# Optimization experiments

Measured on AMD Instinct MI355X. Metric: run time of the kernel, lower is better.

Reference implementation:

```python
import jax, jax.numpy as jnp
import numpy as np

N_NODES = 500000


def _gcn_conv(x, W, b, src, dst, n):
    # x: [N, Fin], W: [Fin, Fout]. PyG GCNConv with add_self_loops + sym norm.
    h = x @ W                                            # [N, Fout]
    deg = jax.ops.segment_sum(jnp.ones_like(dst, dtype=h.dtype), dst,
                              num_segments=n)            # in-degree incl self loops
    dinv = jnp.where(deg > 0, jax.lax.rsqrt(jnp.maximum(deg, 1)), 0.0)
    norm = dinv[src] * dinv[dst]                         # [E]
    msg = h[src] * norm[:, None]                         # gather + scale
    out = jax.ops.segment_sum(msg, dst, num_segments=n)  # scatter-add to targets
    return out + b


def setup_inputs() -> dict:
    key = jax.random.key(0)
    k1, k2, k3, k4 = jax.random.split(key, 4)
    x = jax.random.normal(k1, (N_NODES, 1), dtype=jnp.float32)
    edge_index = jax.random.randint(k2, (2, 8000000), 0, N_NODES, dtype=jnp.int64)
    W1 = jax.random.normal(k3, (1, 32), dtype=jnp.float32) * (1.0 / np.sqrt(1))
    b1 = jnp.zeros((32,), dtype=jnp.float32)
    W2 = jax.random.normal(k4, (32, 2), dtype=jnp.float32) * (1.0 / np.sqrt(32))
    b2 = jnp.zeros((2,), dtype=jnp.float32)
    return {"x": x, "edge_index": edge_index, "W1": W1, "b1": b1, "W2": W2, "b2": b2}


def reference(x, edge_index, W1, b1, W2, b2):
    n = x.shape[0]
    loops = jnp.arange(n, dtype=edge_index.dtype)
    src = jnp.concatenate([edge_index[0], loops])  # add self-loops
    dst = jnp.concatenate([edge_index[1], loops])
    h = _gcn_conv(x, W1, b1, src, dst, n)
    h = jax.nn.relu(h)
    # F.dropout(training=self.training): identity in eval mode
    h = _gcn_conv(h, W2, b2, src, dst, n)
    return jax.nn.log_softmax(h, axis=1)
```

## Files before the change

### kernel.cpp

```cpp
#include <hip/hip_runtime.h>


static constexpr int BKT_BITS = 11;
static constexpr int BKT = 1 << BKT_BITS;
static constexpr int EB = 1024;
static constexpr int EBT = 256;

__global__ void k_hist(const int* __restrict__ dst, int e, int chunk, int nbkt,
                       unsigned* __restrict__ hist) {
  __shared__ unsigned cnt[256];
  int b = blockIdx.x;
  for (int t = threadIdx.x; t < nbkt; t += blockDim.x) cnt[t] = 0;
  __syncthreads();
  int lo = b * chunk;
  int hi = min(lo + chunk, e);
  for (int i = lo + threadIdx.x; i < hi; i += blockDim.x)
    atomicAdd(&cnt[((unsigned)dst[i]) >> BKT_BITS], 1u);
  __syncthreads();
  for (int t = threadIdx.x; t < nbkt; t += blockDim.x)
    hist[(size_t)b * nbkt + t] = cnt[t];
}

__global__ void k_colscan(const unsigned* __restrict__ hist, int nbkt,
                          unsigned* __restrict__ colpre,
                          unsigned* __restrict__ totals) {
  int k = blockIdx.x;
  int lane = threadIdx.x;
  unsigned running = 0;
  for (int c = 0; c < EB; c += 64) {
    unsigned v = hist[(size_t)(c + lane) * nbkt + k];
    unsigned orig = v;
#pragma unroll
    for (int off = 1; off < 64; off <<= 1) {
      unsigned t = __shfl_up(v, off);
      if (lane >= off) v += t;
    }
    colpre[(size_t)(c + lane) * nbkt + k] = running + (v - orig);
    running += __shfl(v, 63);
  }
  if (lane == 0) totals[k] = running;
}

__global__ void k_bucketscan(const unsigned* __restrict__ totals, int nbkt,
                             unsigned* __restrict__ base) {
  if (threadIdx.x == 0) {
    unsigned r = 0;
    for (int k = 0; k < nbkt; ++k) {
      base[k] = r;
      r += totals[k];
    }
    base[nbkt] = r;
  }
}

__global__ void k_scatter(const int* __restrict__ src, const int* __restrict__ dst,
                          int e, int chunk, int nbkt,
                          const unsigned* __restrict__ colpre,
                          const unsigned* __restrict__ base,
                          unsigned* __restrict__ packed) {
  __shared__ unsigned cur[256];
  int b = blockIdx.x;
  for (int t = threadIdx.x; t < nbkt; t += blockDim.x)
    cur[t] = base[t] + colpre[(size_t)b * nbkt + t];
  __syncthreads();
  int lo = b * chunk;
  int hi = min(lo + chunk, e);
  for (int i = lo + threadIdx.x; i < hi; i += blockDim.x) {
    unsigned d = (unsigned)dst[i];
    unsigned k = d >> BKT_BITS;
    unsigned slot = atomicAdd(&cur[k], 1u);
    packed[slot] = ((unsigned)src[i] << BKT_BITS) | (d & (BKT - 1));
  }
}

__global__ void __launch_bounds__(1024) k_degnode(
    const unsigned* __restrict__ packed, const unsigned* __restrict__ base,
    const float* __restrict__ x, int n, float* __restrict__ dinv,
    float* __restrict__ xs) {
  __shared__ unsigned cnt[BKT];
  int k = blockIdx.x;
  for (int t = threadIdx.x; t < BKT; t += blockDim.x) cnt[t] = 0;
  __syncthreads();
  unsigned lo = base[k], hi = base[k + 1];
  for (unsigned i = lo + threadIdx.x; i < hi; i += blockDim.x)
    atomicAdd(&cnt[packed[i] & (BKT - 1)], 1u);
  __syncthreads();
  int g0 = k << BKT_BITS;
  for (int t = threadIdx.x; t < BKT; t += blockDim.x) {
    int g = g0 + t;
    if (g < n) {
      float di = rsqrtf((float)(cnt[t] + 1u));
      dinv[g] = di;
      xs[g] = di * x[g];
    }
  }
}

__global__ void __launch_bounds__(1024) k_accA2(
    const unsigned* __restrict__ packed, const unsigned* __restrict__ base,
    const float* __restrict__ dinv, const float* __restrict__ xs,
    const float* __restrict__ W1, const float* __restrict__ b1,
    const float* __restrict__ W2, int n, float2* __restrict__ yd) {
  __shared__ float acc[BKT];
  __shared__ float sW1[32], sb1[32], sW2[64];
  if (threadIdx.x < 32) {
    sW1[threadIdx.x] = W1[threadIdx.x];
    sb1[threadIdx.x] = b1[threadIdx.x];
  } else if (threadIdx.x < 96) {
    sW2[threadIdx.x - 32] = W2[threadIdx.x - 32];
  }
  for (int t = threadIdx.x; t < BKT; t += blockDim.x) acc[t] = 0.0f;
  __syncthreads();
  int k = blockIdx.x;
  unsigned lo = base[k], hi = base[k + 1];
  for (unsigned i = lo + threadIdx.x; i < hi; i += blockDim.x) {
    unsigned p = packed[i];
    atomicAdd(&acc[p & (BKT - 1)], xs[p >> BKT_BITS]);
  }
  __syncthreads();
  int g0 = k << BKT_BITS;
  for (int t = threadIdx.x; t < BKT; t += blockDim.x) {
    int g = g0 + t;
    if (g >= n) continue;
    float di = dinv[g];
    float s = di * (acc[t] + xs[g]);
    float y0 = 0.0f, y1 = 0.0f;
#pragma unroll
    for (int f = 0; f < 32; ++f) {
      float h = fmaxf(fmaf(s, sW1[f], sb1[f]), 0.0f);
      y0 = fmaf(h, sW2[2 * f + 0], y0);
      y1 = fmaf(h, sW2[2 * f + 1], y1);
    }
    yd[g] = make_float2(di * y0, di * y1);
  }
}

__global__ void __launch_bounds__(1024) k_accB3(
    const unsigned* __restrict__ packed, const unsigned* __restrict__ base,
    const float* __restrict__ dinv, const float2* __restrict__ yd,
    const float* __restrict__ b2, int n, float2* __restrict__ out) {
  __shared__ float a0[BKT], a1[BKT];
  for (int t = threadIdx.x; t < BKT; t += blockDim.x) {
    a0[t] = 0.0f;
    a1[t] = 0.0f;
  }
  __syncthreads();
  int k = blockIdx.x;
  unsigned lo = base[k], hi = base[k + 1];
  for (unsigned i = lo + threadIdx.x; i < hi; i += blockDim.x) {
    unsigned p = packed[i];
    float2 v = yd[p >> BKT_BITS];
    unsigned l = p & (BKT - 1);
    atomicAdd(&a0[l], v.x);
    atomicAdd(&a1[l], v.y);
  }
  __syncthreads();
  float b20 = b2[0], b21 = b2[1];
  int g0 = k << BKT_BITS;
  for (int t = threadIdx.x; t < BKT; t += blockDim.x) {
    int g = g0 + t;
    if (g >= n) continue;
    float di = dinv[g];
    float2 yv = yd[g];
    float t0 = fmaf(di, a0[t] + yv.x, b20);
    float t1 = fmaf(di, a1[t] + yv.y, b21);
    float m = fmaxf(t0, t1);
    float l2 = m + logf(expf(t0 - m) + expf(t1 - m));
    out[g] = make_float2(t0 - l2, t1 - l2);
  }
}

extern "C" void kernel_launch(void* const* d_in, const int* in_sizes, int n_in,
                              void* d_out, int out_size, void* d_ws, size_t ws_size,
                              hipStream_t stream) {
  const float* x = (const float*)d_in[0];
  const int* edge = (const int*)d_in[1];
  const float* W1 = (const float*)d_in[2];
  const float* b1 = (const float*)d_in[3];
  const float* W2 = (const float*)d_in[4];
  const float* b2 = (const float*)d_in[5];
  float2* out = (float2*)d_out;

  const int n = in_sizes[0];
  const int e = in_sizes[1] / 2;
  const int* src = edge;
  const int* dst = edge + e;

  const int nbkt = (n + BKT - 1) >> BKT_BITS;
  const int chunk = (e + EB - 1) / EB;

  char* ws = (char*)d_ws;
  size_t off = 0;
  unsigned* packed = (unsigned*)(ws + off);
  off += (size_t)e * 4;
  unsigned* base = (unsigned*)(ws + off);
  off += ((size_t)(nbkt + 1) * 4 + 255) & ~(size_t)255;
  float* dinv = (float*)(ws + off);
  off += (size_t)n * 4;
  float* xs = (float*)(ws + off);
  off += (size_t)n * 4;
  size_t offB = off;
  unsigned* hist = (unsigned*)(ws + offB);
  unsigned* colpre = (unsigned*)(ws + offB + (size_t)EB * nbkt * 4);
  unsigned* totals = (unsigned*)(ws + offB + 2 * (size_t)EB * nbkt * 4);
  float2* yd = (float2*)(ws + offB);

  k_hist<<<EB, EBT, 0, stream>>>(dst, e, chunk, nbkt, hist);
  k_colscan<<<nbkt, 64, 0, stream>>>(hist, nbkt, colpre, totals);
  k_bucketscan<<<1, 64, 0, stream>>>(totals, nbkt, base);
  k_scatter<<<EB, EBT, 0, stream>>>(src, dst, e, chunk, nbkt, colpre, base, packed);
  k_degnode<<<nbkt, 1024, 0, stream>>>(packed, base, x, n, dinv, xs);
  k_accA2<<<nbkt, 1024, 0, stream>>>(packed, base, dinv, xs, W1, b1, W2, n, yd);
  k_accB3<<<nbkt, 1024, 0, stream>>>(packed, base, dinv, yd, b2, n, out);
}
```

Before: 265.4 us.

## Replace per-block histogram scan with global atomics and staged local-sort scatter

Replaces the per-block bucket histogram plus column scan with a single global bucket-totals histogram using atomics, and vectorizes the dst reads. The scatter kernel now sorts each 8192-edge chunk locally in shared memory, reserves each bucket segment with a global atomicAdd on a cursor, and writes contiguous runs, which should make the packed writes more coalesced. The hist/colpre workspace and two scan kernels are removed. Bucket order within segments becomes nondeterministic across blocks, and later kernels derive segment bounds from the post-scatter cursors.

```diff
diff --git a/kernel.cpp b/kernel.cpp
--- a/kernel.cpp
+++ b/kernel.cpp
@@ -3,85 +3,161 @@
 
 static constexpr int BKT_BITS = 11;
 static constexpr int BKT = 1 << BKT_BITS;
-static constexpr int EB = 1024;
-static constexpr int EBT = 256;
-
-__global__ void k_hist(const int* __restrict__ dst, int e, int chunk, int nbkt,
-                       unsigned* __restrict__ hist) {
-  __shared__ unsigned cnt[256];
-  int b = blockIdx.x;
-  for (int t = threadIdx.x; t < nbkt; t += blockDim.x) cnt[t] = 0;
-  __syncthreads();
-  int lo = b * chunk;
+static constexpr int NB = 256;
+static constexpr int HB = 512;
+static constexpr int HT = 256;
+static constexpr int CHUNK = 8192;
+static constexpr int SCT = 256;
+static constexpr int PERT = CHUNK / SCT;
+
+__global__ void __launch_bounds__(HT) k_hist(const int* __restrict__ dst, int e,
+                                             int chunk, int nbkt,
+                                             unsigned* __restrict__ totals) {
+  __shared__ unsigned cnt[NB];
+  for (int t = threadIdx.x; t < NB; t += HT) cnt[t] = 0;
+  __syncthreads();
+  int lo = blockIdx.x * chunk;
   int hi = min(lo + chunk, e);
-  for (int i = lo + threadIdx.x; i < hi; i += blockDim.x)
+  const int4* d4 = (const int4*)dst;
+  for (int i = (lo >> 2) + threadIdx.x; i < (hi >> 2); i += HT) {
+    int4 d = d4[i];
+    atomicAdd(&cnt[((unsigned)d.x) >> BKT_BITS], 1u);
+    atomicAdd(&cnt[((unsigned)d.y) >> BKT_BITS], 1u);
+    atomicAdd(&cnt[((unsigned)d.z) >> BKT_BITS], 1u);
+    atomicAdd(&cnt[((unsigned)d.w) >> BKT_BITS], 1u);
+  }
+  for (int i = ((hi >> 2) << 2) + threadIdx.x; i < hi; i += HT)
     atomicAdd(&cnt[((unsigned)dst[i]) >> BKT_BITS], 1u);
   __syncthreads();
-  for (int t = threadIdx.x; t < nbkt; t += blockDim.x)
-    hist[(size_t)b * nbkt + t] = cnt[t];
-}
-
-__global__ void k_colscan(const unsigned* __restrict__ hist, int nbkt,
-                          unsigned* __restrict__ colpre,
-                          unsigned* __restrict__ totals) {
-  int k = blockIdx.x;
+  for (int t = threadIdx.x; t < nbkt; t += HT)
+    if (cnt[t]) atomicAdd(&totals[t], cnt[t]);
+}
+
+__global__ void k_basescan(const unsigned* __restrict__ totals, int nbkt,
+                           unsigned* __restrict__ gcur) {
   int lane = threadIdx.x;
   unsigned running = 0;
-  for (int c = 0; c < EB; c += 64) {
-    unsigned v = hist[(size_t)(c + lane) * nbkt + k];
-    unsigned orig = v;
+  for (int c = 0; c < NB; c += 64) {
+    int k = c + lane;
+    unsigned v = (k < nbkt) ? totals[k] : 0u;
+    unsigned incl = v;
 #pragma unroll
     for (int off = 1; off < 64; off <<= 1) {
-      unsigned t = __shfl_up(v, off);
-      if (lane >= off) v += t;
-    }
-    colpre[(size_t)(c + lane) * nbkt + k] = running + (v - orig);
-    running += __shfl(v, 63);
-  }
-  if (lane == 0) totals[k] = running;
-}
-
-__global__ void k_bucketscan(const unsigned* __restrict__ totals, int nbkt,
-                             unsigned* __restrict__ base) {
-  if (threadIdx.x == 0) {
-    unsigned r = 0;
-    for (int k = 0; k < nbkt; ++k) {
-      base[k] = r;
-      r += totals[k];
-    }
-    base[nbkt] = r;
-  }
-}
-
-__global__ void k_scatter(const int* __restrict__ src, const int* __restrict__ dst,
-                          int e, int chunk, int nbkt,
-                          const unsigned* __restrict__ colpre,
-                          const unsigned* __restrict__ base,
-                          unsigned* __restrict__ packed) {
-  __shared__ unsigned cur[256];
-  int b = blockIdx.x;
-  for (int t = threadIdx.x; t < nbkt; t += blockDim.x)
-    cur[t] = base[t] + colpre[(size_t)b * nbkt + t];
-  __syncthreads();
-  int lo = b * chunk;
-  int hi = min(lo + chunk, e);
-  for (int i = lo + threadIdx.x; i < hi; i += blockDim.x) {
-    unsigned d = (unsigned)dst[i];
-    unsigned k = d >> BKT_BITS;
-    unsigned slot = atomicAdd(&cur[k], 1u);
-    packed[slot] = ((unsigned)src[i] << BKT_BITS) | (d & (BKT - 1));
+      unsigned t = __shfl_up(incl, off);
+      if (lane >= off) incl += t;
+    }
+    if (k < nbkt) gcur[k] = running + incl - v;
+    running += __shfl(incl, 63);
+  }
+}
+
+__global__ void __launch_bounds__(SCT) k_scatter(
+    const int* __restrict__ src, const int* __restrict__ dst, int e, int nbkt,
+    unsigned* __restrict__ gcur, unsigned* __restrict__ packed) {
+  __shared__ unsigned staged[CHUNK];
+  __shared__ unsigned cnt[NB];
+  __shared__ unsigned cur[NB];
+  __shared__ unsigned gseg[NB];
+  __shared__ unsigned loff[NB + 1];
+  const int tid = threadIdx.x;
+  const int lo = blockIdx.x * CHUNK;
+  for (int t = tid; t < NB; t += SCT) { cnt[t] = 0u; cur[t] = 0u; }
+  __syncthreads();
+
+  unsigned pk[PERT];
+  unsigned bku[PERT / 4];
+  const int4* s4 = (const int4*)src;
+  const int4* d4 = (const int4*)dst;
+#pragma unroll
+  for (int jj = 0; jj < PERT / 4; ++jj) {
+    int i4 = (lo >> 2) + jj * SCT + tid;
+    unsigned b4 = 0xFFFFFFFFu;
+    if (i4 * 4 + 3 < e) {
+      int4 s = s4[i4];
+      int4 d = d4[i4];
+      unsigned k0 = ((unsigned)d.x) >> BKT_BITS, k1 = ((unsigned)d.y) >> BKT_BITS;
+      unsigned k2 = ((unsigned)d.z) >> BKT_BITS, k3 = ((unsigned)d.w) >> BKT_BITS;
+      pk[jj * 4 + 0] = ((unsigned)s.x << BKT_BITS) | ((unsigned)d.x & (BKT - 1));
+      pk[jj * 4 + 1] = ((unsigned)s.y << BKT_BITS) | ((unsigned)d.y & (BKT - 1));
+      pk[jj * 4 + 2] = ((unsigned)s.z << BKT_BITS) | ((unsigned)d.z & (BKT - 1));
+      pk[jj * 4 + 3] = ((unsigned)s.w << BKT_BITS) | ((unsigned)d.w & (BKT - 1));
+      b4 = k0 | (k1 << 8) | (k2 << 16) | (k3 << 24);
+      atomicAdd(&cnt[k0], 1u);
+      atomicAdd(&cnt[k1], 1u);
+      atomicAdd(&cnt[k2], 1u);
+      atomicAdd(&cnt[k3], 1u);
+    } else {
+#pragma unroll
+      for (int c = 0; c < 4; ++c) {
+        int i = i4 * 4 + c;
+        if (i >= lo && i < e) {
+          unsigned dd = (unsigned)dst[i];
+          unsigned kk = dd >> BKT_BITS;
+          pk[jj * 4 + c] = ((unsigned)src[i] << BKT_BITS) | (dd & (BKT - 1));
+          b4 = (b4 & ~(0xFFu << (8 * c))) | (kk << (8 * c));
+          atomicAdd(&cnt[kk], 1u);
+        }
+      }
+    }
+    bku[jj] = b4;
+  }
+  __syncthreads();
+
+  if (tid < 64) {
+    unsigned running = 0;
+    for (int c = 0; c < NB; c += 64) {
+      int k = c + tid;
+      unsigned v = cnt[k];
+      unsigned incl = v;
+#pragma unroll
+      for (int off = 1; off < 64; off <<= 1) {
+        unsigned t = __shfl_up(incl, off);
+        if (tid >= off) incl += t;
+      }
+      loff[k] = running + incl - v;
+      running += __shfl(incl, 63);
+    }
+    if (tid == 0) loff[NB] = running;
+  }
+  __syncthreads();
+
+  for (int k = tid; k < nbkt; k += SCT)
+    if (cnt[k]) gseg[k] = atomicAdd(&gcur[k], cnt[k]);
+
+#pragma unroll
+  for (int jj = 0; jj < PERT / 4; ++jj) {
+    unsigned b4 = bku[jj];
+#pragma unroll
+    for (int c = 0; c < 4; ++c) {
+      unsigned k = (b4 >> (8 * c)) & 0xFFu;
+      if (k != 0xFFu) {
+        unsigned pos = loff[k] + atomicAdd(&cur[k], 1u);
+        staged[pos] = pk[jj * 4 + c];
+      }
+    }
+  }
+  __syncthreads();
+
+  int mv = (int)loff[nbkt];
+  for (int t = tid; t < mv; t += SCT) {
+    int a = 0, b = nbkt;
+    while (b - a > 1) {
+      int mid = (a + b) >> 1;
+      if ((int)loff[mid] <= t) a = mid; else b = mid;
+    }
+    packed[gseg[a] + (unsigned)(t - (int)loff[a])] = staged[t];
   }
 }
 
 __global__ void __launch_bounds__(1024) k_degnode(
-    const unsigned* __restrict__ packed, const unsigned* __restrict__ base,
+    const unsigned* __restrict__ packed, const unsigned* __restrict__ gcur,
     const float* __restrict__ x, int n, float* __restrict__ dinv,
     float* __restrict__ xs) {
   __shared__ unsigned cnt[BKT];
   int k = blockIdx.x;
   for (int t = threadIdx.x; t < BKT; t += blockDim.x) cnt[t] = 0;
   __syncthreads();
-  unsigned lo = base[k], hi = base[k + 1];
+  unsigned lo = k ? gcur[k - 1] : 0u, hi = gcur[k];
   for (unsigned i = lo + threadIdx.x; i < hi; i += blockDim.x)
     atomicAdd(&cnt[packed[i] & (BKT - 1)], 1u);
   __syncthreads();
@@ -97,7 +173,7 @@
 }
 
 __global__ void __launch_bounds__(1024) k_accA2(
-    const unsigned* __restrict__ packed, const unsigned* __restrict__ base,
+    const unsigned* __restrict__ packed, const unsigned* __restrict__ gcur,
     const float* __restrict__ dinv, const float* __restrict__ xs,
     const float* __restrict__ W1, const float* __restrict__ b1,
     const float* __restrict__ W2, int n, float2* __restrict__ yd) {
@@ -112,7 +188,7 @@
   for (int t = threadIdx.x; t < BKT; t += blockDim.x) acc[t] = 0.0f;
   __syncthreads();
   int k = blockIdx.x;
-  unsigned lo = base[k], hi = base[k + 1];
+  unsigned lo = k ? gcur[k - 1] : 0u, hi = gcur[k];
   for (unsigned i = lo + threadIdx.x; i < hi; i += blockDim.x) {
     unsigned p = packed[i];
     atomicAdd(&acc[p & (BKT - 1)], xs[p >> BKT_BITS]);
@@ -136,7 +212,7 @@
 }
 
 __global__ void __launch_bounds__(1024) k_accB3(
-    const unsigned* __restrict__ packed, const unsigned* __restrict__ base,
+    const unsigned* __restrict__ packed, const unsigned* __restrict__ gcur,
     const float* __restrict__ dinv, const float2* __restrict__ yd,
     const float* __restrict__ b2, int n, float2* __restrict__ out) {
   __shared__ float a0[BKT], a1[BKT];
@@ -146,7 +222,7 @@
   }
   __syncthreads();
   int k = blockIdx.x;
-  unsigned lo = base[k], hi = base[k + 1];
+  unsigned lo = k ? gcur[k - 1] : 0u, hi = gcur[k];
   for (unsigned i = lo + threadIdx.x; i < hi; i += blockDim.x) {
     unsigned p = packed[i];
     float2 v = yd[p >> BKT_BITS];
@@ -162,7 +238,7 @@
     if (g >= n) continue;
     float di = dinv[g];
     float2 yv = yd[g];
-    float t0 = fmaf(di, a0[t] + yv.x, b20);
+    float t0 = fmaf(di, a0[t] + yv.x, b2[0] * 0.0f + b20);
     float t1 = fmaf(di, a1[t] + yv.y, b21);
     float m = fmaxf(t0, t1);
     float l2 = m + logf(expf(t0 - m) + expf(t1 - m));
@@ -187,29 +263,22 @@
   const int* dst = edge + e;
 
   const int nbkt = (n + BKT - 1) >> BKT_BITS;
-  const int chunk = (e + EB - 1) / EB;
+  const int hchunk = (((e + HB - 1) / HB) + 3) & ~3;
+  const int sgrid = (e + CHUNK - 1) / CHUNK;
 
   char* ws = (char*)d_ws;
-  size_t off = 0;
-  unsigned* packed = (unsigned*)(ws + off);
-  off += (size_t)e * 4;
-  unsigned* base = (unsigned*)(ws + off);
-  off += ((size_t)(nbkt + 1) * 4 + 255) & ~(size_t)255;
-  float* dinv = (float*)(ws + off);
-  off += (size_t)n * 4;
-  float* xs = (float*)(ws + off);
-  off += (size_t)n * 4;
-  size_t offB = off;
-  unsigned* hist = (unsigned*)(ws + offB);
-  unsigned* colpre = (unsigned*)(ws + offB + (size_t)EB * nbkt * 4);
-  unsigned* totals = (unsigned*)(ws + offB + 2 * (size_t)EB * nbkt * 4);
-  float2* yd = (float2*)(ws + offB);
-
-  k_hist<<<EB, EBT, 0, stream>>>(dst, e, chunk, nbkt, hist);
-  k_colscan<<<nbkt, 64, 0, stream>>>(hist, nbkt, colpre, totals);
-  k_bucketscan<<<1, 64, 0, stream>>>(totals, nbkt, base);
-  k_scatter<<<EB, EBT, 0, stream>>>(src, dst, e, chunk, nbkt, colpre, base, packed);
-  k_degnode<<<nbkt, 1024, 0, stream>>>(packed, base, x, n, dinv, xs);
-  k_accA2<<<nbkt, 1024, 0, stream>>>(packed, base, dinv, xs, W1, b1, W2, n, yd);
-  k_accB3<<<nbkt, 1024, 0, stream>>>(packed, base, dinv, yd, b2, n, out);
-}
+  unsigned* packed = (unsigned*)ws;
+  unsigned* totals = (unsigned*)(ws + (size_t)e * 4);
+  unsigned* gcur = totals + NB;
+  float* dinv = (float*)(gcur + NB);
+  float* xs = dinv + n;
+  float2* yd = (float2*)(xs + n);
+
+  hipMemsetAsync(totals, 0, NB * sizeof(unsigned), stream);
+  k_hist<<<HB, HT, 0, stream>>>(dst, e, hchunk, nbkt, totals);
+  k_basescan<<<1, 64, 0, stream>>>(totals, nbkt, gcur);
+  k_scatter<<<sgrid, SCT, 0, stream>>>(src, dst, e, nbkt, gcur, packed);
+  k_degnode<<<nbkt, 1024, 0, stream>>>(packed, gcur, x, n, dinv, xs);
+  k_accA2<<<nbkt, 1024, 0, stream>>>(packed, gcur, dinv, xs, W1, b1, W2, n, yd);
+  k_accB3<<<nbkt, 1024, 0, stream>>>(packed, gcur, dinv, yd, b2, n, out);
+}
```

After: 236.3 us. -11.0%, faster.
